# Optimization experiments

Measured on AMD Instinct MI355X. Metric: run time of the kernel, lower is better.

## Reference

```python
import jax, jax.numpy as jnp
import numpy as np

N = 8192
NFEAT = 256
NHID = 64


def setup_inputs() -> dict:
    key = jax.random.key(0)
    k1, k2, k3, k4, k5 = jax.random.split(key, 5)
    x = jax.random.normal(k1, (N, NFEAT), dtype=jnp.float32)
    # symmetric-normalized-ish dense adjacency (random sparse-like weights)
    adj = jax.random.uniform(k2, (N, N), dtype=jnp.float32)
    W1 = jax.random.normal(k3, (NFEAT, NHID), dtype=jnp.float32) * (1.0 / np.sqrt(NFEAT))
    W2 = jax.random.normal(k4, (NHID, NHID), dtype=jnp.float32) * (1.0 / np.sqrt(NHID))
    W3 = jax.random.normal(k5, (NHID, NHID), dtype=jnp.float32) * (1.0 / np.sqrt(NHID))
    return {"x": x, "adj": adj, "W1": W1, "W2": W2, "W3": W3}


def _gcn(x, adj, W):
    # eval mode: dropout is identity. support = x @ W ; out = adj @ support
    return adj @ (x @ W)


def reference(x, adj, W1, W2, W3):
    h1 = jax.nn.relu(_gcn(x, adj, W1))         # [N, nhid]
    mu = _gcn(h1, adj, W2)                      # [N, nhid]
    logvar = _gcn(h1, adj, W3)                  # [N, nhid]
    z = mu                                      # eval: reparameterize returns mu
    recon = z @ z.T                             # [N, N] inner-product decode, act=identity
    return recon, mu, logvar
```

## Files before the change

### kernel.cpp

```cpp
#include <hip/hip_runtime.h>

typedef __bf16 bf16;
typedef __attribute__((ext_vector_type(4))) __bf16 bf16x4;
typedef __attribute__((ext_vector_type(8))) __bf16 bf16x8;
typedef __attribute__((ext_vector_type(4))) float f32x4;

#define MFMA16(a, b, c) __builtin_amdgcn_mfma_f32_16x16x32_bf16((a), (b), (c), 0, 0, 0)

constexpr int N   = 8192;
constexpr int HID = 64;

template <int EPI>
__global__ __launch_bounds__(256) void gcn_adj(const float* __restrict__ A,
                                               const bf16* __restrict__ Bt,
                                               bf16* __restrict__ outT,
                                               const bf16* __restrict__ W23T,
                                               float* __restrict__ mu,
                                               float* __restrict__ lv) {
  __shared__ bf16  As[4][16 * 256];
  __shared__ float Hred[4][16][68];
  __shared__ float Ht[16][72];
  const int tid = threadIdx.x, lane = tid & 63, w = tid >> 6;
  const int r = lane & 15, hi = lane >> 4;
  const int i0 = blockIdx.x * 16;
  const int kb0 = w * 2048;
  constexpr int NSC = 8;

  float4 ra[2][16];
  bf16x8 rb[2][8];
  f32x4 acc[4] = {};

  auto loadChunk = [&](float4 (&dst)[16], int c) {
    const int k0 = kb0 + c * 256;
#pragma unroll
    for (int i = 0; i < 16; ++i)
      dst[i] = *reinterpret_cast<const float4*>(&A[(size_t)(i0 + i) * N + k0 + lane * 4]);
  };
  auto loadB = [&](bf16x8 (&dst)[8], int T) {
    const int k0 = kb0 + T * 64;
#pragma unroll
    for (int n = 0; n < 4; ++n)
#pragma unroll
      for (int kk = 0; kk < 2; ++kk)
        dst[n * 2 + kk] = *reinterpret_cast<const bf16x8*>(
            &Bt[(size_t)(n * 16 + r) * N + k0 + kk * 32 + hi * 8]);
  };
  auto writeChunk = [&](const float4 (&src)[16]) {
    char* base = (char*)&As[w][0];
    const int cl = lane >> 1, bsub = (lane & 1) * 8;
#pragma unroll
    for (int i = 0; i < 16; ++i) {
      bf16x4 o;
      o[0] = (bf16)src[i].x; o[1] = (bf16)src[i].y;
      o[2] = (bf16)src[i].z; o[3] = (bf16)src[i].w;
      *reinterpret_cast<bf16x4*>(base + i * 512 + (cl ^ (i & 7)) * 16 + bsub) = o;
    }
  };
  auto computeTile = [&](int tt, const bf16x8 (&rbv)[8]) {
    const char* base = (const char*)&As[w][0];
#pragma unroll
    for (int kk = 0; kk < 2; ++kk) {
      const int phys = (tt * 8 + kk * 4 + hi) ^ (r & 7);
      const bf16x8 fa = *reinterpret_cast<const bf16x8*>(base + r * 512 + phys * 16);
#pragma unroll
      for (int n = 0; n < 4; ++n)
        acc[n] = MFMA16(fa, rbv[n * 2 + kk], acc[n]);
    }
  };

  loadChunk(ra[0], 0);
  loadChunk(ra[1], 1);
  loadB(rb[0], 0);
  loadB(rb[1], 1);
  writeChunk(ra[0]);

#pragma unroll
  for (int c = 0; c < NSC; ++c) {
#pragma unroll
    for (int tt = 0; tt < 4; ++tt) {
      const int T = c * 4 + tt;
      computeTile(tt, rb[T & 1]);
      if (T + 2 < NSC * 4) loadB(rb[T & 1], T + 2);
    }
    if (c + 1 < NSC) writeChunk(ra[(c + 1) & 1]);
    if (c + 2 < NSC) loadChunk(ra[c & 1], c + 2);
  }

#pragma unroll
  for (int n = 0; n < 4; ++n)
#pragma unroll
    for (int g = 0; g < 4; ++g)
      Hred[w][hi * 4 + g][n * 16 + r] = acc[n][g];
  __syncthreads();
  {
    const int row = tid >> 4, c4 = (tid & 15) * 4;
    float4 s = {0.f, 0.f, 0.f, 0.f};
#pragma unroll
    for (int q = 0; q < 4; ++q) {
      const float4 v = *reinterpret_cast<const float4*>(&Hred[q][row][c4]);
      s.x += v.x; s.y += v.y; s.z += v.z; s.w += v.w;
    }
    if (EPI == 1) {
      s.x = fmaxf(s.x, 0.f); s.y = fmaxf(s.y, 0.f);
      s.z = fmaxf(s.z, 0.f); s.w = fmaxf(s.w, 0.f);
    }
    *reinterpret_cast<float4*>(&Ht[row][c4]) = s;
  }
  __syncthreads();

  if constexpr (EPI == 1) {
    const int j = tid >> 2, iq = tid & 3;
    bf16x4 o;
#pragma unroll
    for (int e = 0; e < 4; ++e) o[e] = (bf16)Ht[iq * 4 + e][j];
    *reinterpret_cast<bf16x4*>(&outT[(size_t)j * N + i0 + iq * 4]) = o;
  } else {
    f32x4 a2[2] = {};
#pragma unroll
    for (int kk = 0; kk < 2; ++kk) {
      const float4 t0 = *reinterpret_cast<const float4*>(&Ht[r][kk * 32 + hi * 8]);
      const float4 t1 = *reinterpret_cast<const float4*>(&Ht[r][kk * 32 + hi * 8 + 4]);
      bf16x8 fa;
      fa[0] = (bf16)t0.x; fa[1] = (bf16)t0.y; fa[2] = (bf16)t0.z; fa[3] = (bf16)t0.w;
      fa[4] = (bf16)t1.x; fa[5] = (bf16)t1.y; fa[6] = (bf16)t1.z; fa[7] = (bf16)t1.w;
#pragma unroll
      for (int j = 0; j < 2; ++j) {
        const int q = w * 2 + j;
        const bf16x8 fw = *reinterpret_cast<const bf16x8*>(
            &W23T[(size_t)(q * 16 + r) * 64 + kk * 32 + hi * 8]);
        a2[j] = MFMA16(fa, fw, a2[j]);
      }
    }
#pragma unroll
    for (int j = 0; j < 2; ++j) {
      const int q = w * 2 + j;
      float* dst = (q < 4) ? mu : lv;
      const int cc = (q & 3) * 16 + r;
#pragma unroll
      for (int g = 0; g < 4; ++g)
        dst[(size_t)(i0 + hi * 4 + g) * HID + cc] = a2[j][g];
    }
  }
}

__global__ __launch_bounds__(256) void gcn_pass0(const float* __restrict__ A, int K,
                                                 const bf16* __restrict__ Bt,
                                                 bf16* __restrict__ outT) {
  __shared__ bf16  As[4][2][16 * 64];
  __shared__ float Hred[4][16][68];
  __shared__ float Ht[16][72];
  const int tid = threadIdx.x, lane = tid & 63, w = tid >> 6;
  const int r = lane & 15, hi = lane >> 4;
  const int i0 = blockIdx.x * 16;
  const int Kw = K >> 2, kb0 = w * Kw, nt = Kw / 64;
  const int aR = hi, aC = r * 4;

  float4 ra[4][4];
  bf16x8 rb[4][8];
  f32x4 acc[4] = {};

  auto loadA = [&](float4 (&dst)[4], int t) {
    const int k0 = kb0 + t * 64;
#pragma unroll
    for (int s = 0; s < 4; ++s)
      dst[s] = *reinterpret_cast<const float4*>(&A[(size_t)(i0 + 4 * s + aR) * K + k0 + aC]);
  };
  auto loadB = [&](bf16x8 (&dst)[8], int t) {
    const int k0 = kb0 + t * 64;
#pragma unroll
    for (int n = 0; n < 4; ++n)
#pragma unroll
      for (int kk = 0; kk < 2; ++kk)
        dst[n * 2 + kk] = *reinterpret_cast<const bf16x8*>(
            &Bt[(size_t)(n * 16 + r) * K + k0 + kk * 32 + hi * 8]);
  };
  auto writeA = [&](int buf, const float4 (&src)[4]) {
    char* base = (char*)&As[w][buf][0];
#pragma unroll
    for (int s = 0; s < 4; ++s) {
      const int R = 4 * s + aR;
      bf16x4 o;
      o[0] = (bf16)src[s].x; o[1] = (bf16)src[s].y;
      o[2] = (bf16)src[s].z; o[3] = (bf16)src[s].w;
      *reinterpret_cast<bf16x4*>(base + R * 128 + ((aC * 2) ^ ((R & 7) << 4))) = o;
    }
  };
  auto compute = [&](int buf, const bf16x8 (&rbv)[8]) {
    const char* base = (const char*)&As[w][buf][0];
#pragma unroll
    for (int kk = 0; kk < 2; ++kk) {
      const bf16x8 fa = *reinterpret_cast<const bf16x8*>(
          base + r * 128 + ((kk * 64 + hi * 16) ^ ((r & 7) << 4)));
#pragma unroll
      for (int n = 0; n < 4; ++n)
        acc[n] = MFMA16(fa, rbv[n * 2 + kk], acc[n]);
    }
  };

  loadA(ra[0], 0);
  loadB(rb[0], 0);
  writeA(0, ra[0]);
  for (int tb = 0; tb < nt; tb += 4) {
#pragma unroll
    for (int u = 0; u < 4; ++u) {
      const int t = tb + u;
      if (t >= nt) continue;
      if (t + 1 < nt) {
        loadA(ra[(u + 1) & 3], t + 1);
        loadB(rb[(u + 1) & 3], t + 1);
        writeA((u + 1) & 1, ra[(u + 1) & 3]);
      }
      compute(u & 1, rb[u & 3]);
    }
  }

#pragma unroll
  for (int n = 0; n < 4; ++n)
#pragma unroll
    for (int g = 0; g < 4; ++g)
      Hred[w][hi * 4 + g][n * 16 + r] = acc[n][g];
  __syncthreads();
  {
    const int row = tid >> 4, c4 = (tid & 15) * 4;
    float4 s = {0.f, 0.f, 0.f, 0.f};
#pragma unroll
    for (int q = 0; q < 4; ++q) {
      const float4 v = *reinterpret_cast<const float4*>(&Hred[q][row][c4]);
      s.x += v.x; s.y += v.y; s.z += v.z; s.w += v.w;
    }
    *reinterpret_cast<float4*>(&Ht[row][c4]) = s;
  }
  __syncthreads();
  const int j = tid >> 2, iq = tid & 3;
  bf16x4 o;
#pragma unroll
  for (int e = 0; e < 4; ++e) o[e] = (bf16)Ht[iq * 4 + e][j];
  *reinterpret_cast<bf16x4*>(&outT[(size_t)j * N + i0 + iq * 4]) = o;
}

__global__ void prep_weights(const float* __restrict__ W1, const float* __restrict__ W2,
                             const float* __restrict__ W3, bf16* __restrict__ W1T,
                             bf16* __restrict__ W23T) {
  const int idx = blockIdx.x * 256 + threadIdx.x;
  if (idx < 16384) {
    const int j = idx >> 8, k = idx & 255;
    W1T[idx] = (bf16)W1[k * HID + j];
  } else {
    const int g = idx - 16384;
    const int j = g >> 6, c = g & 63;
    W23T[g] = (bf16)(j < 64 ? W2[c * HID + j] : W3[c * HID + (j - 64)]);
  }
}

constexpr int LDT = 72;
__global__ __launch_bounds__(256) void recon_mm(const float* __restrict__ mu,
                                                float* __restrict__ out) {
  __shared__ alignas(16) char pool[128 * LDT * 2 * 2];
  bf16* Am = (bf16*)pool;
  bf16* Bm = (bf16*)(pool + 128 * LDT * 2);
  float* Ct = (float*)pool;
  const int tid = threadIdx.x, lane = tid & 63, wave = tid >> 6;
  const int i0 = blockIdx.x * 128, j0 = blockIdx.y * 128;
  {
    const int rr = tid >> 4, c4 = tid & 15;
#pragma unroll
    for (int s = 0; s < 8; ++s) {
      const int row = rr + s * 16;
      const float4 v = *reinterpret_cast<const float4*>(&mu[(size_t)(i0 + row) * HID + c4 * 4]);
      bf16x4 o;
      o[0] = (bf16)v.x; o[1] = (bf16)v.y; o[2] = (bf16)v.z; o[3] = (bf16)v.w;
      *reinterpret_cast<bf16x4*>(&Am[row * LDT + c4 * 4]) = o;
      const float4 u = *reinterpret_cast<const float4*>(&mu[(size_t)(j0 + row) * HID + c4 * 4]);
      bf16x4 p;
      p[0] = (bf16)u.x; p[1] = (bf16)u.y; p[2] = (bf16)u.z; p[3] = (bf16)u.w;
      *reinterpret_cast<bf16x4*>(&Bm[row * LDT + c4 * 4]) = p;
    }
  }
  __syncthreads();
  f32x4 acc[2][8] = {};
  const int rA = wave * 32 + (lane & 15);
#pragma unroll
  for (int kk = 0; kk < 2; ++kk) {
    const int kb = kk * 32 + ((lane >> 4) << 3);
    const bf16x8 a0 = *reinterpret_cast<const bf16x8*>(&Am[rA * LDT + kb]);
    const bf16x8 a1 = *reinterpret_cast<const bf16x8*>(&Am[(rA + 16) * LDT + kb]);
#pragma unroll
    for (int n = 0; n < 8; ++n) {
      const bf16x8 b = *reinterpret_cast<const bf16x8*>(&Bm[(n * 16 + (lane & 15)) * LDT + kb]);
      acc[0][n] = MFMA16(a0, b, acc[0][n]);
      acc[1][n] = MFMA16(a1, b, acc[1][n]);
    }
  }
  const int r4 = (lane >> 4) << 2, c = lane & 15;
#pragma unroll
  for (int h = 0; h < 2; ++h) {
    __syncthreads();
    if ((wave >> 1) == h) {
      const int rbase = (wave & 1) * 32;
#pragma unroll
      for (int m = 0; m < 2; ++m)
#pragma unroll
        for (int n = 0; n < 8; ++n)
#pragma unroll
          for (int g = 0; g < 4; ++g)
            Ct[(rbase + m * 16 + r4 + g) * 132 + n * 16 + c] = acc[m][n][g];
    }
    __syncthreads();
#pragma unroll
    for (int s = 0; s < 8; ++s) {
      const int idx = tid + s * 256;
      const int row = idx >> 5, q = idx & 31;
      const float4 v = *reinterpret_cast<const float4*>(&Ct[row * 132 + q * 4]);
      *reinterpret_cast<float4*>(&out[(size_t)(i0 + h * 64 + row) * N + j0 + q * 4]) = v;
    }
  }
}

extern "C" void kernel_launch(void* const* d_in, const int* in_sizes, int n_in, void* d_out,
                              int out_size, void* d_ws, size_t ws_size, hipStream_t stream) {
  const float* x   = (const float*)d_in[0];
  const float* adj = (const float*)d_in[1];
  const float* W1  = (const float*)d_in[2];
  const float* W2  = (const float*)d_in[3];
  const float* W3  = (const float*)d_in[4];

  float* out    = (float*)d_out;
  float* recon  = out;
  float* mu_out = out + (size_t)N * N;
  float* lv_out = mu_out + (size_t)N * HID;

  char* scr   = (char*)d_out;
  bf16* S1T   = (bf16*)(scr + 0);
  bf16* h1T   = (bf16*)(scr + (1u << 20));
  bf16* W1T   = (bf16*)(scr + (2u << 20));
  bf16* W23T  = (bf16*)(scr + (2u << 20) + 65536);

  prep_weights<<<96, 256, 0, stream>>>(W1, W2, W3, W1T, W23T);
  gcn_pass0<<<512, 256, 0, stream>>>(x, 256, W1T, S1T);
  gcn_adj<1><<<512, 256, 0, stream>>>(adj, S1T, h1T, nullptr, nullptr, nullptr);
  gcn_adj<2><<<512, 256, 0, stream>>>(adj, h1T, nullptr, W23T, mu_out, lv_out);
  recon_mm<<<dim3(64, 64), 256, 0, stream>>>(mu_out, recon);
}
```

Before: 249.3 us.

## Pre-convert adjacency to bf16 once and load MFMA operands directly

Adds a conversion kernel that writes a bf16 copy of the fp32 adjacency into scratch. Both adjacency passes then read this half-size copy, loading A fragments straight into registers instead of staging through LDS. This removes repeated fp32 reads and in-kernel conversion, but adds a full extra read-and-write pass over the matrix.

```diff
diff --git a/kernel.cpp b/kernel.cpp
--- a/kernel.cpp
+++ b/kernel.cpp
@@ -10,34 +10,48 @@
 constexpr int N   = 8192;
 constexpr int HID = 64;
 
+__global__ __launch_bounds__(256) void convert_adj(const float* __restrict__ in,
+                                                   bf16* __restrict__ out) {
+  const size_t stride = (size_t)gridDim.x * 256;
+  const size_t nchunk = (size_t)N * N / 8;
+  for (size_t c = (size_t)blockIdx.x * 256 + threadIdx.x; c < nchunk; c += stride) {
+    const f32x4 v0 = __builtin_nontemporal_load(reinterpret_cast<const f32x4*>(&in[c * 8]));
+    const f32x4 v1 = __builtin_nontemporal_load(reinterpret_cast<const f32x4*>(&in[c * 8 + 4]));
+    bf16x8 o;
+    o[0] = (bf16)v0[0]; o[1] = (bf16)v0[1]; o[2] = (bf16)v0[2]; o[3] = (bf16)v0[3];
+    o[4] = (bf16)v1[0]; o[5] = (bf16)v1[1]; o[6] = (bf16)v1[2]; o[7] = (bf16)v1[3];
+    *reinterpret_cast<bf16x8*>(&out[c * 8]) = o;
+  }
+}
+
 template <int EPI>
-__global__ __launch_bounds__(256) void gcn_adj(const float* __restrict__ A,
-                                               const bf16* __restrict__ Bt,
-                                               bf16* __restrict__ outT,
-                                               const bf16* __restrict__ W23T,
-                                               float* __restrict__ mu,
-                                               float* __restrict__ lv) {
-  __shared__ bf16  As[4][16 * 256];
+__global__ __launch_bounds__(256) void gcn_adjB(const bf16* __restrict__ A,
+                                                const bf16* __restrict__ Bt,
+                                                bf16* __restrict__ outT,
+                                                const bf16* __restrict__ W23T,
+                                                float* __restrict__ mu,
+                                                float* __restrict__ lv) {
   __shared__ float Hred[4][16][68];
   __shared__ float Ht[16][72];
   const int tid = threadIdx.x, lane = tid & 63, w = tid >> 6;
   const int r = lane & 15, hi = lane >> 4;
   const int i0 = blockIdx.x * 16;
   const int kb0 = w * 2048;
-  constexpr int NSC = 8;
-
-  float4 ra[2][16];
-  bf16x8 rb[2][8];
+  constexpr int nt = 32;
+
+  bf16x8 ra[4][2];
+  bf16x8 rb[4][8];
   f32x4 acc[4] = {};
 
-  auto loadChunk = [&](float4 (&dst)[16], int c) {
-    const int k0 = kb0 + c * 256;
-#pragma unroll
-    for (int i = 0; i < 16; ++i)
-      dst[i] = *reinterpret_cast<const float4*>(&A[(size_t)(i0 + i) * N + k0 + lane * 4]);
-  };
-  auto loadB = [&](bf16x8 (&dst)[8], int T) {
-    const int k0 = kb0 + T * 64;
+  auto loadA = [&](bf16x8 (&dst)[2], int t) {
+    const int k0 = kb0 + t * 64;
+#pragma unroll
+    for (int kk = 0; kk < 2; ++kk)
+      dst[kk] = *reinterpret_cast<const bf16x8*>(
+          &A[(size_t)(i0 + r) * N + k0 + kk * 32 + hi * 8]);
+  };
+  auto loadB = [&](bf16x8 (&dst)[8], int t) {
+    const int k0 = kb0 + t * 64;
 #pragma unroll
     for (int n = 0; n < 4; ++n)
 #pragma unroll
@@ -45,45 +59,28 @@
         dst[n * 2 + kk] = *reinterpret_cast<const bf16x8*>(
             &Bt[(size_t)(n * 16 + r) * N + k0 + kk * 32 + hi * 8]);
   };
-  auto writeChunk = [&](const float4 (&src)[16]) {
-    char* base = (char*)&As[w][0];
-    const int cl = lane >> 1, bsub = (lane & 1) * 8;
-#pragma unroll
-    for (int i = 0; i < 16; ++i) {
-      bf16x4 o;
-      o[0] = (bf16)src[i].x; o[1] = (bf16)src[i].y;
-      o[2] = (bf16)src[i].z; o[3] = (bf16)src[i].w;
-      *reinterpret_cast<bf16x4*>(base + i * 512 + (cl ^ (i & 7)) * 16 + bsub) = o;
-    }
-  };
-  auto computeTile = [&](int tt, const bf16x8 (&rbv)[8]) {
-    const char* base = (const char*)&As[w][0];
-#pragma unroll
-    for (int kk = 0; kk < 2; ++kk) {
-      const int phys = (tt * 8 + kk * 4 + hi) ^ (r & 7);
-      const bf16x8 fa = *reinterpret_cast<const bf16x8*>(base + r * 512 + phys * 16);
+  auto compute = [&](const bf16x8 (&av)[2], const bf16x8 (&bv)[8]) {
+#pragma unroll
+    for (int kk = 0; kk < 2; ++kk)
 #pragma unroll
       for (int n = 0; n < 4; ++n)
-        acc[n] = MFMA16(fa, rbv[n * 2 + kk], acc[n]);
-    }
-  };
-
-  loadChunk(ra[0], 0);
-  loadChunk(ra[1], 1);
-  loadB(rb[0], 0);
-  loadB(rb[1], 1);
-  writeChunk(ra[0]);
-
-#pragma unroll
-  for (int c = 0; c < NSC; ++c) {
-#pragma unroll
-    for (int tt = 0; tt < 4; ++tt) {
-      const int T = c * 4 + tt;
-      computeTile(tt, rb[T & 1]);
-      if (T + 2 < NSC * 4) loadB(rb[T & 1], T + 2);
-    }
-    if (c + 1 < NSC) writeChunk(ra[(c + 1) & 1]);
-    if (c + 2 < NSC) loadChunk(ra[c & 1], c + 2);
+        acc[n] = MFMA16(av[kk], bv[n * 2 + kk], acc[n]);
+  };
+
+  loadA(ra[0], 0); loadB(rb[0], 0);
+  loadA(ra[1], 1); loadB(rb[1], 1);
+  loadA(ra[2], 2); loadB(rb[2], 2);
+
+  for (int tb = 0; tb < nt; tb += 4) {
+#pragma unroll
+    for (int u = 0; u < 4; ++u) {
+      const int t = tb + u;
+      if (t + 3 < nt) {
+        loadA(ra[(u + 3) & 3], t + 3);
+        loadB(rb[(u + 3) & 3], t + 3);
+      }
+      compute(ra[u & 3], rb[u & 3]);
+    }
   }
 
 #pragma unroll
@@ -334,10 +331,12 @@
   bf16* h1T   = (bf16*)(scr + (1u << 20));
   bf16* W1T   = (bf16*)(scr + (2u << 20));
   bf16* W23T  = (bf16*)(scr + (2u << 20) + 65536);
-
+  bf16* adjB  = (bf16*)(scr + (64u << 20));
+
+  convert_adj<<<2048, 256, 0, stream>>>(adj, adjB);
   prep_weights<<<96, 256, 0, stream>>>(W1, W2, W3, W1T, W23T);
   gcn_pass0<<<512, 256, 0, stream>>>(x, 256, W1T, S1T);
-  gcn_adj<1><<<512, 256, 0, stream>>>(adj, S1T, h1T, nullptr, nullptr, nullptr);
-  gcn_adj<2><<<512, 256, 0, stream>>>(adj, h1T, nullptr, W23T, mu_out, lv_out);
+  gcn_adjB<1><<<512, 256, 0, stream>>>(adjB, S1T, h1T, nullptr, nullptr, nullptr);
+  gcn_adjB<2><<<512, 256, 0, stream>>>(adjB, h1T, nullptr, W23T, mu_out, lv_out);
   recon_mm<<<dim3(64, 64), 256, 0, stream>>>(mu_out, recon);
 }
```

Result: slower. 275.7 us (+10.6%).
